# Optimization experiments

Measured on AMD Instinct MI355X. Metric: run time of the kernel, lower is better.

## Reference

```python
import jax, jax.numpy as jnp
import numpy as np

EPS = 1e-5

def chan_layernorm(x, g):
    # LayerNorm over channel dim (-3), unbiased=False variance, learned scale g [C]
    mean = jnp.mean(x, axis=1, keepdims=True)
    var = jnp.var(x, axis=1, keepdims=True)
    return (x - mean) * jax.lax.rsqrt(var + EPS) * g[None, :, None, None]

def conv1x1(x, w):
    # w: [out_c, in_c]; pointwise conv == channel GEMM
    return jnp.einsum('bchw,oc->bohw', x, w)

def dwconv3x3(x, w):
    # depthwise 3x3, padding=1; w: [C, 1, 3, 3]
    C = x.shape[1]
    return jax.lax.conv_general_dilated(
        x, w, window_strides=(1, 1), padding='SAME',
        feature_group_count=C,
        dimension_numbers=('NCHW', 'OIHW', 'NCHW'))

def setup_inputs() -> dict:
    key = jax.random.key(0)
    ks = jax.random.split(key, 8)
    b, dim, x, y = 8, 512, 64, 64
    s1 = (dim ** -0.5) * 0.5  # modest init scale
    sd = (9 ** -0.5)
    return {
        'fmap': jax.random.normal(ks[0], (b, dim, x, y), jnp.float32),
        'g': jnp.ones((dim,), jnp.float32),
        'wq1': jax.random.normal(ks[1], (dim, dim), jnp.float32) * s1,
        'wq_dw': jax.random.normal(ks[2], (dim, 1, 3, 3), jnp.float32) * sd,
        'wk1': jax.random.normal(ks[3], (dim, dim), jnp.float32) * s1,
        'wk_dw': jax.random.normal(ks[4], (dim, 1, 3, 3), jnp.float32) * sd,
        'wv1': jax.random.normal(ks[5], (dim, dim), jnp.float32) * s1,
        'wv_dw': jax.random.normal(ks[6], (dim, 1, 3, 3), jnp.float32) * sd,
        'w_out': jax.random.normal(ks[7], (dim, dim), jnp.float32) * s1,
    }

def reference(fmap, g, wq1, wq_dw, wk1, wk_dw, wv1, wv_dw, w_out):
    b, dim, x, y = fmap.shape
    h = 8
    d = dim // h
    scale = d ** -0.5

    fm = chan_layernorm(fmap, g)
    q = dwconv3x3(conv1x1(fm, wq1), wq_dw)
    k = dwconv3x3(conv1x1(fm, wk1), wk_dw)
    v = dwconv3x3(conv1x1(fm, wv1), wv_dw)

    # b (h c) x y -> (b h) (x y) c
    def split_heads(t):
        return t.reshape(b, h, d, x * y).transpose(0, 1, 3, 2).reshape(b * h, x * y, d)
    q, k, v = map(split_heads, (q, k, v))

    q = jax.nn.softmax(q, axis=-1) * scale  # softmax over feature dim
    k = jax.nn.softmax(k, axis=-2)          # softmax over token dim

    ctx = jnp.einsum('bnd,bne->bde', k, v)  # [bh, d, d]
    out = jnp.einsum('bnd,bde->bne', q, ctx)  # [bh, n, d]

    # (b h) (x y) d -> b (h d) x y
    out = out.reshape(b, h, x * y, d).transpose(0, 1, 3, 2).reshape(b, h * d, x, y)
    out = jax.nn.silu(out)
    return conv1x1(out, w_out)
```

## Files before the change

kernel.cpp:

```cpp
#include <hip/hip_runtime.h>
#include <hip/hip_bf16.h>

typedef __attribute__((ext_vector_type(8))) short short8;
typedef __attribute__((ext_vector_type(4))) short shortx4;
typedef __attribute__((ext_vector_type(4))) float floatx4;

#define NB 8
#define C 512
#define NSP 4096
#define NHD 8
#define HDD 64
#define KVPARTS 8

using bf16 = __hip_bfloat16;

__device__ __forceinline__ float b2f(bf16 v) { return __bfloat162float(v); }
__device__ __forceinline__ bf16 f2b(float f) { return __float2bfloat16(f); }
__device__ __forceinline__ float s2f(short s) {
    union { float f; unsigned u; } cv; cv.u = ((unsigned)(unsigned short)s) << 16; return cv.f;
}
__device__ __forceinline__ short f2s(float f) {
    bf16 b = f2b(f); return *reinterpret_cast<short*>(&b);
}

__device__ __forceinline__ void gl2lds16(const bf16* g, bf16* l) {
#if __has_builtin(__builtin_amdgcn_global_load_lds)
    __builtin_amdgcn_global_load_lds(
        (const __attribute__((address_space(1))) unsigned int*)g,
        (__attribute__((address_space(3))) unsigned int*)l, 16, 0, 0);
#else
    *(short8*)l = *(const short8*)g;
#endif
}

__global__ void detect_dtype(const unsigned* __restrict__ g_raw, int* __restrict__ flag) {
    *flag = (g_raw[0] == 0x3F800000u) ? 1 : 0;
}

__global__ __launch_bounds__(256) void prep_w(const void* g, const void* w1q, const void* wdq,
                                              const void* w1k, const void* wdk,
                                              const void* w1v, const void* wdv, const void* w1o,
                                              bf16* gc, bf16* wqkv, bf16* woutc,
                                              bf16* wkdc, bf16* wvdc, bf16* wqdT,
                                              const int* flag) {
    int i = blockIdx.x * 256 + threadIdx.x;
    int f = *flag;
    auto cv = [&](const void* s, int j) -> bf16 {
        return f ? f2b(((const float*)s)[j]) : ((const bf16*)s)[j];
    };
    if (i < C * C) {
        wqkv[i] = cv(w1q, i);
        wqkv[C * C + i] = cv(w1k, i);
        wqkv[2 * C * C + i] = cv(w1v, i);
        woutc[i] = cv(w1o, i);
    }
    if (i < C * 9) {
        int c = i / 9, t = i - c * 9;
        wqdT[t * C + c] = cv(wdq, i);
        wkdc[i] = cv(wdk, i);
        wvdc[i] = cv(wdv, i);
    }
    if (i < C) gc[i] = cv(g, i);
}

__global__ __launch_bounds__(256) void ln_fused(const void* __restrict__ fmap,
                                                const bf16* __restrict__ gc,
                                                bf16* __restrict__ fm,
                                                const int* __restrict__ flag) {
    const int P = 516;
    __shared__ bf16 T[32 * P];
    __shared__ float stat[32][2];
    int b = blockIdx.y;
    int n0 = blockIdx.x * 32;
    int t = threadIdx.x;
    if (*flag) {
        int nq = t & 7;
        int c0 = t >> 3;
        const float* src = (const float*)fmap + (size_t)b * C * NSP + n0 + nq * 4;
#pragma unroll 4
        for (int it = 0; it < 16; ++it) {
            int c = c0 + it * 32;
            float4 v = *(const float4*)(src + (size_t)c * NSP);
            T[(nq * 4 + 0) * P + c] = f2b(v.x);
            T[(nq * 4 + 1) * P + c] = f2b(v.y);
            T[(nq * 4 + 2) * P + c] = f2b(v.z);
            T[(nq * 4 + 3) * P + c] = f2b(v.w);
        }
    } else {
        int nq = t & 3;
        int c0 = t >> 2;
        const bf16* src = (const bf16*)fmap + (size_t)b * C * NSP + n0 + nq * 8;
#pragma unroll 4
        for (int it = 0; it < 8; ++it) {
            int c = c0 + it * 64;
            union { short8 s; short h[8]; } v;
            v.s = *(const short8*)(src + (size_t)c * NSP);
#pragma unroll
            for (int j = 0; j < 8; ++j)
                *(short*)&T[(nq * 8 + j) * P + c] = v.h[j];
        }
    }
    __syncthreads();
    int n = t >> 3, part = t & 7;
    {
        float s = 0.f, sq = 0.f;
        const bf16* row = T + n * P + part * 64;
#pragma unroll
        for (int i = 0; i < 8; ++i) {
            union { short8 v; short h[8]; } u;
            u.v = *(const short8*)(row + i * 8);
#pragma unroll
            for (int j = 0; j < 8; ++j) { float x = s2f(u.h[j]); s += x; sq += x * x; }
        }
#pragma unroll
        for (int off = 1; off < 8; off <<= 1) {
            s += __shfl_xor(s, off, 64);
            sq += __shfl_xor(sq, off, 64);
        }
        if (part == 0) {
            float mean = s * (1.f / C);
            float var = sq * (1.f / C) - mean * mean;
            stat[n][0] = mean;
            stat[n][1] = rsqrtf(var + 1e-5f);
        }
    }
    __syncthreads();
    float mean = stat[n][0], rs = stat[n][1];
    bf16* dst = fm + ((size_t)b * NSP + n0 + n) * C + part * 64;
    const bf16* row = T + n * P + part * 64;
    const bf16* gp = gc + part * 64;
#pragma unroll
    for (int i = 0; i < 8; ++i) {
        union { short8 v; short h[8]; } u, gv, ov;
        u.v = *(const short8*)(row + i * 8);
        gv.v = *(const short8*)(gp + i * 8);
#pragma unroll
        for (int j = 0; j < 8; ++j)
            ov.h[j] = f2s((s2f(u.h[j]) - mean) * rs * s2f(gv.h[j]));
        *(short8*)(dst + i * 8) = ov.v;
    }
}

template <int PHASE>
__global__ __launch_bounds__(512, 2) void gemm256(const bf16* __restrict__ X,
                                                  const bf16* __restrict__ Wall,
                                                  void* __restrict__ O0,
                                                  void* __restrict__ O1,
                                                  void* __restrict__ O2,
                                                  const int* __restrict__ flag) {
    __shared__ __align__(16) bf16 SH[4][256 * 64];
    bf16* SA0 = SH[0];
    bf16* SA1 = SH[1];
    bf16* SB0 = SH[2];
    bf16* SB1 = SH[3];
    const int nbase = blockIdx.x * 256;
    const int obase = blockIdx.y * 256;
    const int b = blockIdx.z;
    const int t = threadIdx.x;
    const int lane = t & 63, w = t >> 6;
    const int wm = w >> 2, wn = w & 3;
    const int m16 = lane & 15, q = lane >> 4;
    const bool AisW = (PHASE == 0) && (obase < 512);
    const bf16* gX = X + (size_t)b * NSP * C + (size_t)nbase * C;
    const bf16* gW = Wall + (size_t)obase * C;
    const bf16* gA = AisW ? gW : gX;
    const bf16* gB = AisW ? gX : gW;

    const int srow = t >> 3;
    const int sch = ((t & 7) ^ (srow & 7)) * 8;

    const int rA = wm * 128 + m16;
    const int rB = wn * 64 + m16;
    const int cs0 = ((q) ^ (m16 & 7)) * 8;
    const int cs1 = ((4 + q) ^ (m16 & 7)) * 8;

    floatx4 acc[8][4] = {};
    short8 Bf[4][2];

#define STAGE(LDS, G, K0, H)                                                   \
    {                                                                          \
        const bf16* _s = (G) + (size_t)((H) * 128 + srow) * C + (K0) + sch;    \
        bf16* _d = (LDS) + (H) * 8192 + t * 8;                                 \
        gl2lds16(_s, _d);                                                      \
        gl2lds16(_s + 64 * C, _d + 4096);                                      \
    }

#define VMW(N)                                                                 \
    {                                                                          \
        asm volatile("s_waitcnt vmcnt(" #N ")" ::: "memory");                  \
        __builtin_amdgcn_sched_barrier(0);                                     \
    }

#define PH(J, LA, LB, LOADB, STAGE_STMT, WAIT_STMT)                            \
    {                                                                          \
        short8 Af0, Af1, Af2, Af3;                                             \
        if (LOADB) {                                                           \
            _Pragma("unroll") for (int nt = 0; nt < 4; ++nt) {                 \
                Bf[nt][0] = *(const short8*)((LB) + (rB + nt * 16) * 64 + cs0);\
                Bf[nt][1] = *(const short8*)((LB) + (rB + nt * 16) * 64 + cs1);\
            }                                                                  \
        }                                                                      \
        Af0 = *(const short8*)((LA) + (rA + (2 * (J)) * 16) * 64 + cs0);       \
        Af1 = *(const short8*)((LA) + (rA + (2 * (J)) * 16) * 64 + cs1);       \
        Af2 = *(const short8*)((LA) + (rA + (2 * (J) + 1) * 16) * 64 + cs0);   \
        Af3 = *(const short8*)((LA) + (rA + (2 * (J) + 1) * 16) * 64 + cs1);   \
        STAGE_STMT;                                                            \
        WAIT_STMT;                                                             \
        __builtin_amdgcn_sched_barrier(0);                                     \
        __builtin_amdgcn_s_barrier();                                          \
        asm volatile("s_waitcnt lgkmcnt(0)" ::: "memory");                     \
        __builtin_amdgcn_sched_barrier(0);                                     \
        __builtin_amdgcn_s_setprio(1);                                         \
        _Pragma("unroll") for (int nt = 0; nt < 4; ++nt) {                     \
            acc[2 * (J)][nt] = __builtin_amdgcn_mfma_f32_16x16x32_bf16(        \
                Af0, Bf[nt][0], acc[2 * (J)][nt], 0, 0, 0);                    \
            acc[2 * (J)][nt] = __builtin_amdgcn_mfma_f32_16x16x32_bf16(        \
                Af1, Bf[nt][1], acc[2 * (J)][nt], 0, 0, 0);                    \
            acc[2 * (J) + 1][nt] = __builtin_amdgcn_mfma_f32_16x16x32_bf16(    \
                Af2, Bf[nt][0], acc[2 * (J) + 1][nt], 0, 0, 0);                \
            acc[2 * (J) + 1][nt] = __builtin_amdgcn_mfma_f32_16x16x32_bf16(    \
                Af3, Bf[nt][1], acc[2 * (J) + 1][nt], 0, 0, 0);                \
        }                                                                      \
        __builtin_amdgcn_s_setprio(0);                                         \
        __builtin_amdgcn_sched_barrier(0);                                     \
        __builtin_amdgcn_s_barrier();                                          \
    }

    STAGE(SA0, gA, 0, 0);
    STAGE(SA0, gA, 0, 1);
    STAGE(SB0, gB, 0, 0);
    STAGE(SB0, gB, 0, 1);
    STAGE(SB1, gB, 64, 0);
    STAGE(SB1, gB, 64, 1);
    VMW(0);
    __builtin_amdgcn_s_barrier();

    for (int i = 0; i < 3; ++i) {
        int kT = i * 128;
        PH(0, SA0, SB0, true,  STAGE(SA1, gA, kT + 64, 0),  ((void)0));
        PH(1, SA0, SB0, false, STAGE(SA1, gA, kT + 64, 1),  ((void)0));
        PH(2, SA0, SB0, false, STAGE(SB0, gB, kT + 128, 0), ((void)0));
        PH(3, SA0, SB0, false, STAGE(SB0, gB, kT + 128, 1), VMW(4));
        PH(0, SA1, SB1, true,  STAGE(SA0, gA, kT + 128, 0), ((void)0));
        PH(1, SA1, SB1, false, STAGE(SA0, gA, kT + 128, 1), ((void)0));
        PH(2, SA1, SB1, false, STAGE(SB1, gB, kT + 192, 0), ((void)0));
        PH(3, SA1, SB1, false, STAGE(SB1, gB, kT + 192, 1), VMW(4));
    }
    PH(0, SA0, SB0, true,  STAGE(SA1, gA, 448, 0), ((void)0));
    PH(1, SA0, SB0, false, STAGE(SA1, gA, 448, 1), ((void)0));
    PH(2, SA0, SB0, false, ((void)0), ((void)0));
    PH(3, SA0, SB0, false, ((void)0), VMW(0));
    PH(0, SA1, SB1, true,  ((void)0), ((void)0));
    PH(1, SA1, SB1, false, ((void)0), ((void)0));
    PH(2, SA1, SB1, false, ((void)0), ((void)0));
    PH(3, SA1, SB1, false, ((void)0), ((void)0));

#undef PH
#undef VMW
#undef STAGE

    if (PHASE == 0 && AisW) {
        bf16* out = (bf16*)O0 + (size_t)b * NSP * C;
#pragma unroll
        for (int nt = 0; nt < 4; ++nt)
#pragma unroll
            for (int mt = 0; mt < 8; ++mt) {
                int n = nbase + wn * 64 + nt * 16 + m16;
                int o = obase + wm * 128 + mt * 16 + q * 4;
                shortx4 pv;
#pragma unroll
                for (int r = 0; r < 4; ++r) pv[r] = f2s(acc[mt][nt][r]);
                *(shortx4*)(out + (size_t)n * C + o) = pv;
            }
    } else if (PHASE == 0) {
        bf16* out = (bf16*)((obase < 1024) ? O1 : O2) + (size_t)b * C * NSP;
        int ob = obase & 511;
#pragma unroll
        for (int nt = 0; nt < 4; ++nt)
#pragma unroll
            for (int mt = 0; mt < 8; ++mt) {
                int o = ob + wn * 64 + nt * 16 + m16;
                int n = nbase + wm * 128 + mt * 16 + q * 4;
                shortx4 pv;
#pragma unroll
                for (int r = 0; r < 4; ++r) pv[r] = f2s(acc[mt][nt][r]);
                *(shortx4*)(out + (size_t)o * NSP + n) = pv;
            }
    } else {
        int is_f32 = *flag;
        size_t outb = (size_t)b * C * NSP;
#pragma unroll
        for (int nt = 0; nt < 4; ++nt)
#pragma unroll
            for (int mt = 0; mt < 8; ++mt) {
                int o = obase + wn * 64 + nt * 16 + m16;
                int n = nbase + wm * 128 + mt * 16 + q * 4;
                size_t off = outb + (size_t)o * NSP + n;
                if (is_f32) {
                    *(floatx4*)((float*)O0 + off) = acc[mt][nt];
                } else {
                    shortx4 pv;
#pragma unroll
                    for (int r = 0; r < 4; ++r) pv[r] = f2s(acc[mt][nt][r]);
                    *(shortx4*)((bf16*)O0 + off) = pv;
                }
            }
    }
}

__device__ __forceinline__ void load_row10(float* v, const bf16* rp0, int yy, int x0) {
    if ((unsigned)yy >= 64u) {
#pragma unroll
        for (int j = 0; j < 10; ++j) v[j] = 0.f;
        return;
    }
    const bf16* rp = rp0 + yy * 64;
    v[0] = (x0 > 0) ? b2f(rp[x0 - 1]) : 0.f;
    union { short8 s; short h[8]; } m;
    m.s = *(const short8*)(rp + x0);
#pragma unroll
    for (int j = 0; j < 8; ++j) v[1 + j] = s2f(m.h[j]);
    v[9] = (x0 < 56) ? b2f(rp[x0 + 8]) : 0.f;
}

__global__ __launch_bounds__(512) void kv_ctx(const bf16* __restrict__ Kpre,
                                              const bf16* __restrict__ Vpre,
                                              const bf16* __restrict__ wkd,
                                              const bf16* __restrict__ wvd,
                                              float* __restrict__ Apart,
                                              float* __restrict__ Zpart) {
    __shared__ __align__(16) bf16 KB[2][64 * 64];
    __shared__ __align__(16) bf16 VB[2][64 * 64];
    const int part = blockIdx.x;
    const int bh = blockIdx.y;
    const int b = bh >> 3, h = bh & 7;
    const int t = threadIdx.x;
    const int ch = t >> 3;
    const int xo = t & 7, x0 = xo * 8;
    const int c = h * 64 + ch;
    const bf16* kp = Kpre + ((size_t)b * C + c) * NSP;
    const bf16* vp = Vpre + ((size_t)b * C + c) * NSP;
    float wk[9], wv[9];
#pragma unroll
    for (int i = 0; i < 9; ++i) { wk[i] = b2f(wkd[c * 9 + i]); wv[i] = b2f(wvd[c * 9 + i]); }
    const int ybase = part * (64 / KVPARTS);
    float k3[3][10], v3[3][10];
    load_row10(k3[0], kp, ybase - 1, x0);
    load_row10(k3[1], kp, ybase, x0);
    load_row10(v3[0], vp, ybase - 1, x0);
    load_row10(v3[1], vp, ybase, x0);
    float zsum = 0.f;
    const int lane = t & 63, w = t >> 6;
    const int et = w >> 1, wd = w & 1;
    const int m16 = lane & 15, q = lane >> 4;
    const int arow = et * 16 + m16;
    const int br0 = wd * 32 + m16;
    floatx4 acc[2] = {};
    for (int yy = 0; yy < 64 / KVPARTS; ++yy) {
        const int buf = yy & 1;
        load_row10(k3[2], kp, ybase + yy + 1, x0);
        load_row10(v3[2], vp, ybase + yy + 1, x0);
        float ak[8] = {}, av[8] = {};
#pragma unroll
        for (int ky = 0; ky < 3; ++ky)
#pragma unroll
            for (int i = 0; i < 8; ++i) {
                ak[i] += wk[ky * 3 + 0] * k3[ky][i] + wk[ky * 3 + 1] * k3[ky][i + 1] + wk[ky * 3 + 2] * k3[ky][i + 2];
                av[i] += wv[ky * 3 + 0] * v3[ky][i] + wv[ky * 3 + 1] * v3[ky][i + 1] + wv[ky * 3 + 2] * v3[ky][i + 2];
            }
        union { short8 s; short h[8]; } ke, ve;
#pragma unroll
        for (int i = 0; i < 8; ++i) {
            float e = __expf(ak[i]);
            zsum += e;
            ke.h[i] = f2s(e);
            ve.h[i] = f2s(av[i]);
        }
        const int chunk = xo ^ (ch & 7);
        *(short8*)(&KB[buf][ch * 64 + chunk * 8]) = ke.s;
        *(short8*)(&VB[buf][ch * 64 + chunk * 8]) = ve.s;
#pragma unroll
        for (int j = 0; j < 10; ++j) {
            k3[0][j] = k3[1][j]; k3[1][j] = k3[2][j];
            v3[0][j] = v3[1][j]; v3[1][j] = v3[2][j];
        }
        __syncthreads();
#pragma unroll
        for (int kh = 0; kh < 2; ++kh) {
            short8 Af = *(const short8*)(&VB[buf][arow * 64 + (((kh * 4 + q) ^ (arow & 7)) * 8)]);
#pragma unroll
            for (int dt = 0; dt < 2; ++dt) {
                int brow = br0 + dt * 16;
                short8 Bfm = *(const short8*)(&KB[buf][brow * 64 + (((kh * 4 + q) ^ (brow & 7)) * 8)]);
                acc[dt] = __builtin_amdgcn_mfma_f32_16x16x32_bf16(Af, Bfm, acc[dt], 0, 0, 0);
            }
        }
    }
#pragma unroll
    for (int off = 1; off < 8; off <<= 1) zsum += __shfl_xor(zsum, off, 64);
    if ((lane & 7) == 0)
        Zpart[((size_t)bh * KVPARTS + part) * 64 + ch] = zsum;
#pragma unroll
    for (int dt = 0; dt < 2; ++dt)
#pragma unroll
        for (int r = 0; r < 4; ++r) {
            int e = et * 16 + q * 4 + r;
            int d = wd * 32 + dt * 16 + m16;
            Apart[(((size_t)bh * KVPARTS + part) * 64 + e) * 64 + d] = acc[dt][r];
        }
}

__global__ __launch_bounds__(256) void kv_fin(const float* __restrict__ Apart,
                                              const float* __restrict__ Zpart,
                                              bf16* __restrict__ ctxb) {
    int bh = blockIdx.x;
    int t = threadIdx.x;
    int e = t >> 2, dq = (t & 3) * 16;
    float z[16] = {}, a[16] = {};
#pragma unroll
    for (int p = 0; p < KVPARTS; ++p) {
        const float* zp = Zpart + ((size_t)bh * KVPARTS + p) * 64 + dq;
        const float* ap = Apart + (((size_t)bh * KVPARTS + p) * 64 + e) * 64 + dq;
#pragma unroll
        for (int j = 0; j < 16; ++j) { z[j] += zp[j]; a[j] += ap[j]; }
    }
    bf16* op = ctxb + ((size_t)bh * 64 + e) * 64 + dq;
#pragma unroll
    for (int j = 0; j < 16; ++j) op[j] = f2b(a[j] / z[j]);
}

__global__ __launch_bounds__(256) void q_attn(const bf16* __restrict__ Qpre,
                                              const bf16* __restrict__ WdT,
                                              const bf16* __restrict__ ctxb,
                                              bf16* __restrict__ O) {
    __shared__ __align__(16) bf16 P[64 * 512];
    __shared__ __align__(16) bf16 CT[8 * 64 * 64];
    const int y = blockIdx.x, b = blockIdx.y;
    const int t = threadIdx.x;
#pragma unroll
    for (int j = 0; j < 16; ++j) {
        int idx = t + j * 256;
        int h = idx >> 9, e = (idx >> 3) & 63, co = idx & 7;
        short8 vv = *(const short8*)(ctxb + (((size_t)(b * 8 + h) * 64 + e) * 64 + co * 8));
        *(short8*)(&CT[h * 4096 + e * 64 + ((co ^ (e & 7)) * 8)]) = vv;
    }
    const int lane = t & 63, wvw = t >> 6;
    const int co = lane;
    const bf16* qp = Qpre + (size_t)b * NSP * C + co * 8;
    union sh8 { short8 s; short h[8]; };
    sh8 w9[9];
#pragma unroll
    for (int tap = 0; tap < 9; ++tap) w9[tap].s = *(const short8*)(WdT + tap * C + co * 8);
    sh8 cw[3][3];
    const int x0 = wvw * 16;
    auto ldc = [&](int ny, int nx) -> short8 {
        if ((unsigned)ny >= 64u || (unsigned)nx >= 64u) { short8 z = {}; return z; }
        return *(const short8*)(qp + (size_t)(ny * 64 + nx) * C);
    };
#pragma unroll
    for (int dy = 0; dy < 3; ++dy) {
        cw[dy][0].s = ldc(y + dy - 1, x0 - 1);
        cw[dy][1].s = ldc(y + dy - 1, x0);
    }
#pragma unroll 2
    for (int xi = 0; xi < 16; ++xi) {
        const int x = x0 + xi;
#pragma unroll
        for (int dy = 0; dy < 3; ++dy) cw[dy][2].s = ldc(y + dy - 1, x + 1);
        float a8[8] = {};
#pragma unroll
        for (int dy = 0; dy < 3; ++dy)
#pragma unroll
            for (int dc = 0; dc < 3; ++dc)
#pragma unroll
                for (int i = 0; i < 8; ++i)
                    a8[i] += s2f(w9[dy * 3 + dc].h[i]) * s2f(cw[dy][dc].h[i]);
        float mx = a8[0];
#pragma unroll
        for (int i = 1; i < 8; ++i) mx = fmaxf(mx, a8[i]);
#pragma unroll
        for (int off = 1; off < 8; off <<= 1) mx = fmaxf(mx, __shfl_xor(mx, off, 64));
        float e8[8], s = 0.f;
#pragma unroll
        for (int i = 0; i < 8; ++i) { e8[i] = __expf(a8[i] - mx); s += e8[i]; }
#pragma unroll
        for (int off = 1; off < 8; off <<= 1) s += __shfl_xor(s, off, 64);
        float inv = 0.125f / s;
        union sh8 pv;
#pragma unroll
        for (int i = 0; i < 8; ++i) pv.h[i] = f2s(e8[i] * inv);
        *(short8*)(&P[x * 512 + ((co ^ (x & 7)) * 8)]) = pv.s;
#pragma unroll
        for (int dy = 0; dy < 3; ++dy) { cw[dy][0] = cw[dy][1]; cw[dy][1] = cw[dy][2]; }
    }
    __syncthreads();
    const int m16 = lane & 15, q = lane >> 4;
    const int nrow = wvw * 16 + m16;
    floatx4 acc[8][4] = {};
#pragma unroll
    for (int kh = 0; kh < 2; ++kh) {
#pragma unroll
        for (int h2 = 0; h2 < 8; ++h2) {
            int lc = h2 * 8 + kh * 4 + q;
            short8 Bfr = *(const short8*)(&P[nrow * 512 + ((lc ^ (nrow & 7)) * 8)]);
#pragma unroll
            for (int et = 0; et < 4; ++et) {
                int erow = et * 16 + m16;
                short8 Afr = *(const short8*)(&CT[h2 * 4096 + erow * 64 + (((kh * 4 + q) ^ (erow & 7)) * 8)]);
                acc[h2][et] = __builtin_amdgcn_mfma_f32_16x16x32_bf16(Afr, Bfr, acc[h2][et], 0, 0, 0);
            }
        }
    }
    bf16* op = O + ((size_t)b * NSP + (size_t)y * 64 + wvw * 16 + m16) * C;
#pragma unroll
    for (int h2 = 0; h2 < 8; ++h2)
#pragma unroll
        for (int et = 0; et < 4; ++et) {
            shortx4 pv;
#pragma unroll
            for (int r = 0; r < 4; ++r) {
                float xv = acc[h2][et][r];
                pv[r] = f2s(xv / (1.f + __expf(-xv)));
            }
            *(shortx4*)(op + h2 * 64 + et * 16 + q * 4) = pv;
        }
}

extern "C" void kernel_launch(void* const* d_in, const int* in_sizes, int n_in,
                              void* d_out, int out_size, void* d_ws, size_t ws_size,
                              hipStream_t stream) {
    char* ws = (char*)d_ws;
    const size_t TB = (size_t)NB * NSP * C * 2;
    bf16* buf0 = (bf16*)(ws);
    bf16* buf1 = (bf16*)(ws + TB);
    bf16* buf2 = (bf16*)(ws + 2 * TB);
    bf16* buf3 = (bf16*)(ws + 3 * TB);
    char* ext = ws + 4 * TB;
    bf16* ctxb  = (bf16*)(ext);                   ext += 524288;
    bf16* gc    = (bf16*)(ext);                   ext += 4096;
    bf16* wqkv  = (bf16*)(ext);                   ext += 3 * C * C * 2;
    bf16* woutc = (bf16*)(ext);                   ext += C * C * 2;
    bf16* wkdc  = (bf16*)(ext);                   ext += 16384;
    bf16* wvdc  = (bf16*)(ext);                   ext += 16384;
    bf16* wqdT  = (bf16*)(ext);                   ext += 16384;
    int*  flag  = (int*)(ext);                    ext += 4096;
    float* Apart = (float*)buf0;
    float* Zpart = Apart + (size_t)NB * NHD * KVPARTS * 64 * 64;

    detect_dtype<<<1, 1, 0, stream>>>((const unsigned*)d_in[1], flag);
    prep_w<<<(C * C + 255) / 256, 256, 0, stream>>>(d_in[1], d_in[2], d_in[3], d_in[4], d_in[5],
                                                    d_in[6], d_in[7], d_in[8],
                                                    gc, wqkv, woutc, wkdc, wvdc, wqdT, flag);

    ln_fused<<<dim3(NSP / 32, NB), 256, 0, stream>>>(d_in[0], gc, buf0, flag);

    gemm256<0><<<dim3(NSP / 256, 6, NB), 512, 0, stream>>>(buf0, wqkv, buf1, buf2, buf3, flag);

    kv_ctx<<<dim3(KVPARTS, NB * NHD), 512, 0, stream>>>(buf2, buf3, wkdc, wvdc, Apart, Zpart);
    kv_fin<<<NB * NHD, 256, 0, stream>>>(Apart, Zpart, ctxb);

    q_attn<<<dim3(64, NB), 256, 0, stream>>>(buf1, wqdT, ctxb, buf2);

    gemm256<1><<<dim3(NSP / 256, C / 256, NB), 512, 0, stream>>>(buf2, woutc, d_out, nullptr, nullptr, flag);
}
```

Measured before the change: 340.9 us.

## Widen q_attn to 512 threads, drop ctx LDS staging, unroll kv loop

q_attn now runs 512 threads per block. Each wave handles 8 x-positions in the depthwise/softmax phase and a 16-row by 4-head tile in the MFMA phase, which halves the per-thread accumulator count. The context matrix is no longer staged in shared memory; MFMA A-fragments are read directly from global memory, with L2 reuse expected. Occupancy hints are raised and the kv_ctx row loop is fully unrolled. The trade-off is global/L2 traffic in the inner MFMA loop and possible register pressure from the unrolling.

```diff
diff --git a/kernel.cpp b/kernel.cpp
--- a/kernel.cpp
+++ b/kernel.cpp
@@ -356,6 +356,7 @@
     const int arow = et * 16 + m16;
     const int br0 = wd * 32 + m16;
     floatx4 acc[2] = {};
+#pragma unroll
     for (int yy = 0; yy < 64 / KVPARTS; ++yy) {
         const int buf = yy & 1;
         load_row10(k3[2], kp, ybase + yy + 1, x0);
@@ -429,30 +430,22 @@
     for (int j = 0; j < 16; ++j) op[j] = f2b(a[j] / z[j]);
 }
 
-__global__ __launch_bounds__(256) void q_attn(const bf16* __restrict__ Qpre,
-                                              const bf16* __restrict__ WdT,
-                                              const bf16* __restrict__ ctxb,
-                                              bf16* __restrict__ O) {
+__global__ __launch_bounds__(512, 4) void q_attn(const bf16* __restrict__ Qpre,
+                                                 const bf16* __restrict__ WdT,
+                                                 const bf16* __restrict__ ctxb,
+                                                 bf16* __restrict__ O) {
     __shared__ __align__(16) bf16 P[64 * 512];
-    __shared__ __align__(16) bf16 CT[8 * 64 * 64];
     const int y = blockIdx.x, b = blockIdx.y;
     const int t = threadIdx.x;
-#pragma unroll
-    for (int j = 0; j < 16; ++j) {
-        int idx = t + j * 256;
-        int h = idx >> 9, e = (idx >> 3) & 63, co = idx & 7;
-        short8 vv = *(const short8*)(ctxb + (((size_t)(b * 8 + h) * 64 + e) * 64 + co * 8));
-        *(short8*)(&CT[h * 4096 + e * 64 + ((co ^ (e & 7)) * 8)]) = vv;
-    }
-    const int lane = t & 63, wvw = t >> 6;
+    const int lane = t & 63, w = t >> 6;
     const int co = lane;
+    const int x0 = w * 8;
     const bf16* qp = Qpre + (size_t)b * NSP * C + co * 8;
     union sh8 { short8 s; short h[8]; };
     sh8 w9[9];
 #pragma unroll
     for (int tap = 0; tap < 9; ++tap) w9[tap].s = *(const short8*)(WdT + tap * C + co * 8);
     sh8 cw[3][3];
-    const int x0 = wvw * 16;
     auto ldc = [&](int ny, int nx) -> short8 {
         if ((unsigned)ny >= 64u || (unsigned)nx >= 64u) { short8 z = {}; return z; }
         return *(const short8*)(qp + (size_t)(ny * 64 + nx) * C);
@@ -462,8 +455,8 @@
         cw[dy][0].s = ldc(y + dy - 1, x0 - 1);
         cw[dy][1].s = ldc(y + dy - 1, x0);
     }
-#pragma unroll 2
-    for (int xi = 0; xi < 16; ++xi) {
+#pragma unroll
+    for (int xi = 0; xi < 8; ++xi) {
         const int x = x0 + xi;
 #pragma unroll
         for (int dy = 0; dy < 3; ++dy) cw[dy][2].s = ldc(y + dy - 1, x + 1);
@@ -495,34 +488,37 @@
     }
     __syncthreads();
     const int m16 = lane & 15, q = lane >> 4;
-    const int nrow = wvw * 16 + m16;
-    floatx4 acc[8][4] = {};
+    const int nt16 = w & 3, hh = w >> 2;
+    const int nrow = nt16 * 16 + m16;
+    const bf16* cb = ctxb + (size_t)b * 8 * 4096;
+    floatx4 acc[4][4] = {};
 #pragma unroll
     for (int kh = 0; kh < 2; ++kh) {
 #pragma unroll
-        for (int h2 = 0; h2 < 8; ++h2) {
+        for (int hi = 0; hi < 4; ++hi) {
+            int h2 = hh * 4 + hi;
             int lc = h2 * 8 + kh * 4 + q;
             short8 Bfr = *(const short8*)(&P[nrow * 512 + ((lc ^ (nrow & 7)) * 8)]);
 #pragma unroll
             for (int et = 0; et < 4; ++et) {
                 int erow = et * 16 + m16;
-                short8 Afr = *(const short8*)(&CT[h2 * 4096 + erow * 64 + (((kh * 4 + q) ^ (erow & 7)) * 8)]);
-                acc[h2][et] = __builtin_amdgcn_mfma_f32_16x16x32_bf16(Afr, Bfr, acc[h2][et], 0, 0, 0);
-            }
-        }
-    }
-    bf16* op = O + ((size_t)b * NSP + (size_t)y * 64 + wvw * 16 + m16) * C;
-#pragma unroll
-    for (int h2 = 0; h2 < 8; ++h2)
+                short8 Afr = *(const short8*)(cb + (size_t)h2 * 4096 + erow * 64 + (kh * 4 + q) * 8);
+                acc[hi][et] = __builtin_amdgcn_mfma_f32_16x16x32_bf16(Afr, Bfr, acc[hi][et], 0, 0, 0);
+            }
+        }
+    }
+    bf16* op = O + ((size_t)b * NSP + (size_t)y * 64 + nt16 * 16 + m16) * C + hh * 256;
+#pragma unroll
+    for (int hi = 0; hi < 4; ++hi)
 #pragma unroll
         for (int et = 0; et < 4; ++et) {
             shortx4 pv;
 #pragma unroll
             for (int r = 0; r < 4; ++r) {
-                float xv = acc[h2][et][r];
+                float xv = acc[hi][et][r];
                 pv[r] = f2s(xv / (1.f + __expf(-xv)));
             }
-            *(shortx4*)(op + h2 * 64 + et * 16 + q * 4) = pv;
+            *(shortx4*)(op + hi * 64 + et * 16 + q * 4) = pv;
         }
 }
 
@@ -559,7 +555,7 @@
     kv_ctx<<<dim3(KVPARTS, NB * NHD), 512, 0, stream>>>(buf2, buf3, wkdc, wvdc, Apart, Zpart);
     kv_fin<<<NB * NHD, 256, 0, stream>>>(Apart, Zpart, ctxb);
 
-    q_attn<<<dim3(64, NB), 256, 0, stream>>>(buf1, wqdT, ctxb, buf2);
+    q_attn<<<dim3(64, NB), 512, 0, stream>>>(buf1, wqdT, ctxb, buf2);
 
     gemm256<1><<<dim3(NSP / 256, C / 256, NB), 512, 0, stream>>>(buf2, woutc, d_out, nullptr, nullptr, flag);
 }
```

New measurement: 448.7 us. 31.6% more time.
